# Kernel optimization log

Hardware: AMD Instinct MI355X
Metric: run time of the kernel (lower is better)

## Reference

```python
import jax, jax.numpy as jnp
import numpy as np

C = 256
HEADS = 8
HD = C // HEADS
SCALE = HD ** -0.5


def conv1x1(x, W, b):
    # x: [B,C_in,H,W], W: [C_out,C_in], b: [C_out]
    return jnp.einsum('oc,bchw->bohw', W, x) + b[None, :, None, None]


def setup_inputs() -> dict:
    key = jax.random.key(0)
    ks = jax.random.split(key, 12)
    B, H, Wd = 2, 48, 48
    s = C ** -0.5
    return {
        'x': jax.random.normal(ks[0], (B, C, H, Wd), jnp.float32),
        'uncertainty': jax.random.uniform(ks[1], (B, 1, H, Wd), jnp.float32),
        'Wq': jax.random.normal(ks[2], (C, C), jnp.float32) * s,
        'bq': jnp.zeros((C,), jnp.float32),
        'Wk': jax.random.normal(ks[3], (C, C), jnp.float32) * s,
        'bk': jnp.zeros((C,), jnp.float32),
        'Wv': jax.random.normal(ks[4], (C, C), jnp.float32) * s,
        'bv': jnp.zeros((C,), jnp.float32),
        'Wg': jax.random.normal(ks[5], (C, 1), jnp.float32),
        'bg': jnp.zeros((C,), jnp.float32),
        'Wo': jax.random.normal(ks[6], (C, C), jnp.float32) * s,
        'bo': jnp.zeros((C,), jnp.float32),
    }


def reference(x, uncertainty, Wq, bq, Wk, bk, Wv, bv, Wg, bg, Wo, bo):
    B, _, H, Wd = x.shape
    N = H * Wd
    # uncertainty gate (1x1 conv from 1 channel to C channels)
    uw = conv1x1(uncertainty, Wg, bg)            # [B,C,H,W]
    gated_x = x * (1.0 - uw)
    q = conv1x1(gated_x, Wq, bq).reshape(B, HEADS, HD, N)
    k = conv1x1(gated_x, Wk, bk).reshape(B, HEADS, HD, N)
    v = conv1x1(x, Wv, bv).reshape(B, HEADS, HD, N)
    # scores: [B,h,N,N] (query tokens n, key tokens m)
    scores = jnp.einsum('bhdn,bhdm->bhnm', q, k) * SCALE
    u_flat = uncertainty.reshape(B, 1, 1, N)      # mask over key axis
    scores = scores * (1.0 - u_flat)
    attn = jax.nn.softmax(scores, axis=-1)
    out = jnp.einsum('bhnm,bhdm->bhdn', attn, v)  # [B,h,hd,N]
    out = out.reshape(B, C, H, Wd)
    out = conv1x1(out, Wo, bo)
    return out + x
```

## Files before the change

kernel.cpp:

```cpp
#include <hip/hip_runtime.h>
#include <hip/hip_bf16.h>

typedef float f32x4 __attribute__((ext_vector_type(4)));
typedef __bf16 bf16x8 __attribute__((ext_vector_type(8)));
typedef __bf16 bf16x4 __attribute__((ext_vector_type(4)));
typedef short s16x4 __attribute__((ext_vector_type(4)));

constexpr int C = 256;
constexpr int N = 2304;
constexpr int T = 2 * N;

#if __has_builtin(__builtin_amdgcn_exp2f)
#define EXP2F(x) __builtin_amdgcn_exp2f(x)
#else
#define EXP2F(x) exp2f(x)
#endif

__device__ __forceinline__ bf16x8 load_bf8(const __bf16* p) {
    return *reinterpret_cast<const bf16x8*>(p);
}

__device__ __forceinline__ f32x4 mfma32(bf16x8 a, bf16x8 b, f32x4 c) {
    return __builtin_amdgcn_mfma_f32_16x16x32_bf16(a, b, c, 0, 0, 0);
}

#if __has_builtin(__builtin_amdgcn_mfma_f32_16x16x16bf16_1k)
__device__ __forceinline__ f32x4 mfma16(bf16x4 a, bf16x4 b, f32x4 c) {
    return __builtin_amdgcn_mfma_f32_16x16x16bf16_1k(
        __builtin_bit_cast(s16x4, a), __builtin_bit_cast(s16x4, b), c, 0, 0, 0);
}
#else
__device__ __forceinline__ f32x4 mfma16(bf16x4 a, bf16x4 b, f32x4 c) {
    f32x4 d;
    asm volatile("v_mfma_f32_16x16x16_bf16 %0, %1, %2, %3"
                 : "=v"(d) : "v"(a), "v"(b), "v"(c));
    return d;
}
#endif

__device__ __forceinline__ void gload_lds16(const __bf16* g, __bf16* l) {
    __builtin_amdgcn_global_load_lds(
        (const __attribute__((address_space(1))) void*)g,
        (__attribute__((address_space(3))) void*)l, 16, 0, 0);
}

#define VMCNT0() asm volatile("s_waitcnt vmcnt(0)" ::: "memory")
#define LGKM0()  asm volatile("s_waitcnt lgkmcnt(0)" ::: "memory")

__global__ void wconv_kernel(const float* __restrict__ Wq, const float* __restrict__ Wk,
                             const float* __restrict__ Wv, const float* __restrict__ Wo,
                             __bf16* __restrict__ Wb) {
    const float* srcs[4] = {Wq, Wk, Wv, Wo};
    int m = blockIdx.x >> 6;
    int idx = (blockIdx.x & 63) * 256 + threadIdx.x;
    float4 v = reinterpret_cast<const float4*>(srcs[m])[idx];
    bf16x4 o = { (__bf16)v.x, (__bf16)v.y, (__bf16)v.z, (__bf16)v.w };
    reinterpret_cast<bf16x4*>(Wb + m * 65536)[idx] = o;
}

__global__ void prep_kernel(const float* __restrict__ x, const float* __restrict__ u,
                            const float* __restrict__ Wg, const float* __restrict__ bg,
                            __bf16* __restrict__ xT, __bf16* __restrict__ gxT) {
    __shared__ float tile[32][65];
    int b = blockIdx.z, c0 = blockIdx.y * 32, n0 = blockIdx.x * 64;
    int t = threadIdx.x;
    const float* xp = x + (b * C + c0) * N + n0;
    #pragma unroll
    for (int r = 0; r < 8; ++r) {
        int cl = r * 4 + (t >> 6);
        int nl = t & 63;
        tile[cl][nl] = xp[cl * N + nl];
    }
    __syncthreads();
    int cq = (t & 7) * 4;
    #pragma unroll
    for (int it = 0; it < 2; ++it) {
        int nl = it * 32 + (t >> 3);
        float uv = u[b * N + n0 + nl];
        bf16x4 xo, go;
        #pragma unroll
        for (int j = 0; j < 4; ++j) {
            int c = c0 + cq + j;
            float xv = tile[cq + j][nl];
            float gate = 1.0f - (Wg[c] * uv + bg[c]);
            xo[j] = (__bf16)xv;
            go[j] = (__bf16)(xv * gate);
        }
        int tok = b * N + n0 + nl;
        *reinterpret_cast<bf16x4*>(xT + (long)tok * C + c0 + cq) = xo;
        *reinterpret_cast<bf16x4*>(gxT + (long)tok * C + c0 + cq) = go;
    }
}

__global__ __launch_bounds__(256) void qkv_kernel(const __bf16* __restrict__ Wb,
    const __bf16* __restrict__ xT, const __bf16* __restrict__ gxT,
    const float* __restrict__ bq, const float* __restrict__ bk, const float* __restrict__ bv,
    const float* __restrict__ u,
    __bf16* __restrict__ Q, __bf16* __restrict__ K, __bf16* __restrict__ V) {
    int proj = blockIdx.z;
    int o0 = blockIdx.y * 64;
    int t0 = blockIdx.x * 32;
    int wave = threadIdx.x >> 6, lane = threadIdx.x & 63;
    int g = lane >> 4, r = lane & 15;
    int ow = o0 + wave * 16;
    const __bf16* W = Wb + proj * 65536;
    const __bf16* inp = (proj == 2) ? xT : gxT;
    f32x4 acc[2] = {};
    for (int k = 0; k < 8; ++k) {
        bf16x8 a = load_bf8(W + (ow + r) * C + k * 32 + g * 8);
        #pragma unroll
        for (int tb = 0; tb < 2; ++tb) {
            bf16x8 bfr = load_bf8(inp + (long)(t0 + tb * 16 + r) * C + k * 32 + g * 8);
            acc[tb] = mfma32(a, bfr, acc[tb]);
        }
    }
    const float* bias = (proj == 0) ? bq : (proj == 1) ? bk : bv;
    float bvw[4];
    #pragma unroll
    for (int i = 0; i < 4; ++i) bvw[i] = bias[ow + g * 4 + i];
    int h = ow >> 5, d0 = (ow & 31) + g * 4;
    const float SC = 0.17677669529663687f * 1.4426950408889634f;
    #pragma unroll
    for (int tb = 0; tb < 2; ++tb) {
        int t = t0 + tb * 16 + r;
        int b = t / N, n = t % N;
        if (proj == 2) {
            #pragma unroll
            for (int i = 0; i < 4; ++i)
                V[((long)(b * 8 + h) * 32 + d0 + i) * N + n] = (__bf16)(acc[tb][i] + bvw[i]);
        } else {
            bf16x4 outv;
            if (proj == 1) {
                float scale = SC * (1.0f - u[t]);
                #pragma unroll
                for (int i = 0; i < 4; ++i) outv[i] = (__bf16)((acc[tb][i] + bvw[i]) * scale);
            } else {
                #pragma unroll
                for (int i = 0; i < 4; ++i) outv[i] = (__bf16)(acc[tb][i] + bvw[i]);
            }
            __bf16* dst = (proj == 0) ? Q : K;
            *reinterpret_cast<bf16x4*>(dst + ((long)(b * 8 + h) * N + n) * 32 + d0) = outv;
        }
    }
}

__global__ __launch_bounds__(256) void attn_kernel(const __bf16* __restrict__ Q,
    const __bf16* __restrict__ K, const __bf16* __restrict__ V,
    __bf16* __restrict__ aoT) {
    __shared__ __bf16 sK[2][2][2048];
    __shared__ __bf16 sV[2][2][2048];
    int id = blockIdx.x;
    int xcd = id & 7, j = id >> 3;
    int bh = xcd + 8 * (j / 72);
    int qblk = j % 72;
    int tid = threadIdx.x;
    int wave = tid >> 6, lane = tid & 63;
    int wp = wave & 1, pair = wave >> 1;
    int g = lane >> 4, r = lane & 15;
    int q0 = qblk * 32;
    const __bf16* Qg = Q + (long)bh * N * 32;
    const __bf16* Kg = K + (long)bh * N * 32 + (long)pair * 1152 * 32;
    const __bf16* Vg = V + (long)bh * 32 * N + pair * 1152;
    bf16x8 qf = load_bf8(Qg + (q0 + wp * 16 + r) * 32 + g * 8);
    long ksrc = (long)(wp * 64 + lane) * 8;
    int rr1 = wp * 8 + (lane >> 3);
    long vsrc0 = (long)rr1 * N + ((lane & 7) ^ ((rr1 >> 1) & 7)) * 8;
    int rr2 = 16 + rr1;
    long vsrc1 = (long)rr2 * N + ((lane & 7) ^ ((rr2 >> 1) & 7)) * 8;
    __bf16* kb0 = &sK[pair][0][0];
    __bf16* kb1 = &sK[pair][1][0];
    __bf16* vb0 = &sV[pair][0][0];
    __bf16* vb1 = &sV[pair][1][0];
    auto STAGE = [&](long m0, __bf16* kd, __bf16* vd) {
        gload_lds16(Kg + m0 * 32 + ksrc,        kd + wp * 512);
        gload_lds16(Kg + m0 * 32 + 1024 + ksrc, kd + 1024 + wp * 512);
        gload_lds16(Vg + vsrc0 + m0,            vd + wp * 512);
        gload_lds16(Vg + vsrc1 + m0,            vd + 1024 + wp * 512);
    };
    bf16x4 onesv;
    #pragma unroll
    for (int i = 0; i < 4; ++i) onesv[i] = (__bf16)1.0f;
    f32x4 oa0 = {}, oa1 = {}, oal = {};
    int k2r = (r >> 1) & 7;
    STAGE(0, kb0, vb0);
    for (int t = 0; t < 18; ++t) {
        LGKM0();
        VMCNT0();
        __builtin_amdgcn_s_barrier();
        const __bf16* kb = (t & 1) ? kb1 : kb0;
        const __bf16* vb = (t & 1) ? vb1 : vb0;
        if (t < 17)
            STAGE((long)(t + 1) * 64, (t & 1) ? kb0 : kb1, (t & 1) ? vb0 : vb1);
        bf16x8 kc0 = load_bf8(kb + (0 * 16 + r) * 32 + g * 8);
        bf16x8 kc1 = load_bf8(kb + (1 * 16 + r) * 32 + g * 8);
        bf16x8 kc2 = load_bf8(kb + (2 * 16 + r) * 32 + g * 8);
        bf16x8 kc3 = load_bf8(kb + (3 * 16 + r) * 32 + g * 8);
        bf16x4 vf[4][2];
        #pragma unroll
        for (int tt = 0; tt < 4; ++tt) {
            int pg = (((tt * 2 + (g >> 1)) ^ k2r) << 1) | (g & 1);
            #pragma unroll
            for (int dt = 0; dt < 2; ++dt)
                vf[tt][dt] = *reinterpret_cast<const bf16x4*>(
                    vb + (dt * 16 + r) * 64 + pg * 4);
        }
        f32x4 z = {};
        __builtin_amdgcn_s_setprio(1);
        f32x4 s0 = mfma32(kc0, qf, z);
        f32x4 s1 = mfma32(kc1, qf, z);
        f32x4 s2 = mfma32(kc2, qf, z);
        f32x4 s3 = mfma32(kc3, qf, z);
        __builtin_amdgcn_s_setprio(0);
        bf16x4 pa0, pa1, pa2, pa3;
        #pragma unroll
        for (int i = 0; i < 4; ++i) pa0[i] = (__bf16)EXP2F(s0[i]);
        #pragma unroll
        for (int i = 0; i < 4; ++i) pa1[i] = (__bf16)EXP2F(s1[i]);
        #pragma unroll
        for (int i = 0; i < 4; ++i) pa2[i] = (__bf16)EXP2F(s2[i]);
        #pragma unroll
        for (int i = 0; i < 4; ++i) pa3[i] = (__bf16)EXP2F(s3[i]);
        __builtin_amdgcn_s_setprio(1);
        oa0 = mfma16(vf[0][0], pa0, oa0);
        oa1 = mfma16(vf[0][1], pa0, oa1);
        oal = mfma16(onesv,    pa0, oal);
        oa0 = mfma16(vf[1][0], pa1, oa0);
        oa1 = mfma16(vf[1][1], pa1, oa1);
        oal = mfma16(onesv,    pa1, oal);
        oa0 = mfma16(vf[2][0], pa2, oa0);
        oa1 = mfma16(vf[2][1], pa2, oa1);
        oal = mfma16(onesv,    pa2, oal);
        oa0 = mfma16(vf[3][0], pa3, oa0);
        oa1 = mfma16(vf[3][1], pa3, oa1);
        oal = mfma16(onesv,    pa3, oal);
        __builtin_amdgcn_s_setprio(0);
    }
    __builtin_amdgcn_s_barrier();
    float* F = reinterpret_cast<float*>(&sK[0][0][0]);
    *reinterpret_cast<f32x4*>(F + wave * 512 + r * 32 + g * 4) = oa0;
    *reinterpret_cast<f32x4*>(F + wave * 512 + r * 32 + 16 + g * 4) = oa1;
    if (g == 0) F[2048 + wave * 16 + r] = oal[0];
    __builtin_amdgcn_s_barrier();
    if (tid < 128) {
        int q = tid >> 2;
        int wpq = q >> 4, qq = q & 15;
        int d8 = (tid & 3) * 8;
        int base0 = wpq * 512 + qq * 32 + d8;
        int base1 = (wpq + 2) * 512 + qq * 32 + d8;
        f32x4 a0 = *reinterpret_cast<f32x4*>(F + base0) +
                   *reinterpret_cast<f32x4*>(F + base1);
        f32x4 a1 = *reinterpret_cast<f32x4*>(F + base0 + 4) +
                   *reinterpret_cast<f32x4*>(F + base1 + 4);
        float l = F[2048 + wpq * 16 + qq] + F[2048 + (wpq + 2) * 16 + qq];
        float inv = 1.0f / l;
        bf16x8 ov;
        #pragma unroll
        for (int i = 0; i < 4; ++i) {
            ov[i] = (__bf16)(a0[i] * inv);
            ov[4 + i] = (__bf16)(a1[i] * inv);
        }
        int b = bh >> 3, h = bh & 7;
        *reinterpret_cast<bf16x8*>(aoT + (long)(b * N + q0 + q) * C + h * 32 + d8) = ov;
    }
}

__global__ __launch_bounds__(256) void outp_kernel(const __bf16* __restrict__ Wb,
    const __bf16* __restrict__ aoT, const float* __restrict__ bo,
    const float* __restrict__ x, float* __restrict__ out) {
    int o0 = blockIdx.y * 64;
    int t0 = blockIdx.x * 16;
    int wave = threadIdx.x >> 6, lane = threadIdx.x & 63;
    int g = lane >> 4, r = lane & 15;
    int ow = o0 + wave * 16;
    const __bf16* W = Wb + 3 * 65536;
    f32x4 acc = {};
    for (int k = 0; k < 8; ++k) {
        bf16x8 a = load_bf8(W + (ow + r) * C + k * 32 + g * 8);
        bf16x8 bfr = load_bf8(aoT + (long)(t0 + r) * C + k * 32 + g * 8);
        acc = mfma32(a, bfr, acc);
    }
    float bvw[4];
    #pragma unroll
    for (int i = 0; i < 4; ++i) bvw[i] = bo[ow + g * 4 + i];
    int t = t0 + r;
    int b = t / N, n = t % N;
    #pragma unroll
    for (int i = 0; i < 4; ++i) {
        long idx = ((long)b * C + ow + g * 4 + i) * N + n;
        out[idx] = acc[i] + bvw[i] + x[idx];
    }
}

extern "C" void kernel_launch(void* const* d_in, const int* in_sizes, int n_in,
                              void* d_out, int out_size, void* d_ws, size_t ws_size,
                              hipStream_t stream) {
    const float* x  = (const float*)d_in[0];
    const float* u  = (const float*)d_in[1];
    const float* Wq = (const float*)d_in[2];
    const float* bq = (const float*)d_in[3];
    const float* Wk = (const float*)d_in[4];
    const float* bk = (const float*)d_in[5];
    const float* Wv = (const float*)d_in[6];
    const float* bv = (const float*)d_in[7];
    const float* Wg = (const float*)d_in[8];
    const float* bg = (const float*)d_in[9];
    const float* Wo = (const float*)d_in[10];
    const float* bo = (const float*)d_in[11];
    float* out = (float*)d_out;

    char* ws = (char*)d_ws;
    size_t off = 0;
    auto alloc = [&](size_t bytes) {
        char* p = ws + off;
        off += (bytes + 255) & ~(size_t)255;
        return p;
    };
    __bf16* Wb  = (__bf16*)alloc((size_t)4 * 65536 * 2);
    __bf16* xT  = (__bf16*)alloc((size_t)T * C * 2);
    __bf16* gxT = (__bf16*)alloc((size_t)T * C * 2);
    __bf16* Qb  = (__bf16*)alloc((size_t)16 * N * 32 * 2);
    __bf16* Kb  = (__bf16*)alloc((size_t)16 * N * 32 * 2);
    __bf16* Vb  = (__bf16*)alloc((size_t)16 * N * 32 * 2);
    __bf16* aoT = (__bf16*)alloc((size_t)T * C * 2);

    wconv_kernel<<<256, 256, 0, stream>>>(Wq, Wk, Wv, Wo, Wb);
    prep_kernel<<<dim3(36, 8, 2), 256, 0, stream>>>(x, u, Wg, bg, xT, gxT);
    qkv_kernel<<<dim3(144, 4, 3), 256, 0, stream>>>(Wb, xT, gxT, bq, bk, bv, u, Qb, Kb, Vb);
    attn_kernel<<<1152, 256, 0, stream>>>(Qb, Kb, Vb, aoT);
    outp_kernel<<<dim3(288, 4), 256, 0, stream>>>(Wb, aoT, bo, x, out);
}
```

Before: 78.76 us.

## Halve attention key tile to 32 and unify swizzled K/V LDS staging

The attention loop now processes 32 keys per iteration instead of 64, doubling the iteration count to 36 and halving the shared memory to 16 KB per block. K and V staging each use a single 16-byte async load per lane with one XOR swizzle shared by both, and the LDS read offsets are precomputed outside the loop. The aim is higher occupancy and fewer LDS bank conflicts. In exchange there are twice as many barriers and waits per block and less MFMA work between synchronisations.

```diff
diff --git a/kernel.cpp b/kernel.cpp
--- a/kernel.cpp
+++ b/kernel.cpp
@@ -147,8 +147,9 @@
 __global__ __launch_bounds__(256) void attn_kernel(const __bf16* __restrict__ Q,
     const __bf16* __restrict__ K, const __bf16* __restrict__ V,
     __bf16* __restrict__ aoT) {
-    __shared__ __bf16 sK[2][2][2048];
-    __shared__ __bf16 sV[2][2][2048];
+    __shared__ __bf16 sMem[8192];
+    __bf16* sK = sMem;
+    __bf16* sV = sMem + 4096;
     int id = blockIdx.x;
     int xcd = id & 7, j = id >> 3;
     int bh = xcd + 8 * (j / 72);
@@ -162,81 +163,62 @@
     const __bf16* Kg = K + (long)bh * N * 32 + (long)pair * 1152 * 32;
     const __bf16* Vg = V + (long)bh * 32 * N + pair * 1152;
     bf16x8 qf = load_bf8(Qg + (q0 + wp * 16 + r) * 32 + g * 8);
-    long ksrc = (long)(wp * 64 + lane) * 8;
-    int rr1 = wp * 8 + (lane >> 3);
-    long vsrc0 = (long)rr1 * N + ((lane & 7) ^ ((rr1 >> 1) & 7)) * 8;
-    int rr2 = 16 + rr1;
-    long vsrc1 = (long)rr2 * N + ((lane & 7) ^ ((rr2 >> 1) & 7)) * 8;
-    __bf16* kb0 = &sK[pair][0][0];
-    __bf16* kb1 = &sK[pair][1][0];
-    __bf16* vb0 = &sV[pair][0][0];
-    __bf16* vb1 = &sV[pair][1][0];
-    auto STAGE = [&](long m0, __bf16* kd, __bf16* vd) {
-        gload_lds16(Kg + m0 * 32 + ksrc,        kd + wp * 512);
-        gload_lds16(Kg + m0 * 32 + 1024 + ksrc, kd + 1024 + wp * 512);
-        gload_lds16(Vg + vsrc0 + m0,            vd + wp * 512);
-        gload_lds16(Vg + vsrc1 + m0,            vd + 1024 + wp * 512);
+    int s_ = wp * 64 + lane;
+    int l_ = s_ ^ ((s_ >> 3) & 7);
+    const __bf16* kSrc = Kg + (l_ >> 2) * 32 + (l_ & 3) * 8;
+    const __bf16* vSrc = Vg + (long)(l_ >> 2) * N + (l_ & 3) * 8;
+    __bf16* kd0 = sK + pair * 2048;
+    __bf16* vd0 = sV + pair * 2048;
+    auto STAGE = [&](long m0, int buf) {
+        gload_lds16(kSrc + m0 * 32, kd0 + buf * 1024 + wp * 512);
+        gload_lds16(vSrc + m0,      vd0 + buf * 1024 + wp * 512);
     };
+    int key = (r >> 1) & 7;
+    int pk0 = ((r * 4 + g) ^ key) * 8;
+    int pk1 = (((16 + r) * 4 + g) ^ key) * 8;
+    int pv00 = (((r) * 4 + 0 + (g >> 1)) ^ key) * 8 + (g & 1) * 4;
+    int pv01 = (((16 + r) * 4 + 0 + (g >> 1)) ^ key) * 8 + (g & 1) * 4;
+    int pv10 = (((r) * 4 + 2 + (g >> 1)) ^ key) * 8 + (g & 1) * 4;
+    int pv11 = (((16 + r) * 4 + 2 + (g >> 1)) ^ key) * 8 + (g & 1) * 4;
     bf16x4 onesv;
     #pragma unroll
     for (int i = 0; i < 4; ++i) onesv[i] = (__bf16)1.0f;
     f32x4 oa0 = {}, oa1 = {}, oal = {};
-    int k2r = (r >> 1) & 7;
-    STAGE(0, kb0, vb0);
-    for (int t = 0; t < 18; ++t) {
+    STAGE(0, 0);
+    for (int t = 0; t < 36; ++t) {
         LGKM0();
         VMCNT0();
         __builtin_amdgcn_s_barrier();
-        const __bf16* kb = (t & 1) ? kb1 : kb0;
-        const __bf16* vb = (t & 1) ? vb1 : vb0;
-        if (t < 17)
-            STAGE((long)(t + 1) * 64, (t & 1) ? kb0 : kb1, (t & 1) ? vb0 : vb1);
-        bf16x8 kc0 = load_bf8(kb + (0 * 16 + r) * 32 + g * 8);
-        bf16x8 kc1 = load_bf8(kb + (1 * 16 + r) * 32 + g * 8);
-        bf16x8 kc2 = load_bf8(kb + (2 * 16 + r) * 32 + g * 8);
-        bf16x8 kc3 = load_bf8(kb + (3 * 16 + r) * 32 + g * 8);
-        bf16x4 vf[4][2];
-        #pragma unroll
-        for (int tt = 0; tt < 4; ++tt) {
-            int pg = (((tt * 2 + (g >> 1)) ^ k2r) << 1) | (g & 1);
-            #pragma unroll
-            for (int dt = 0; dt < 2; ++dt)
-                vf[tt][dt] = *reinterpret_cast<const bf16x4*>(
-                    vb + (dt * 16 + r) * 64 + pg * 4);
-        }
+        const __bf16* kb = kd0 + (t & 1) * 1024;
+        const __bf16* vb = vd0 + (t & 1) * 1024;
+        if (t < 35) STAGE((long)(t + 1) * 32, (t & 1) ^ 1);
+        bf16x8 kc0 = load_bf8(kb + pk0);
+        bf16x8 kc1 = load_bf8(kb + pk1);
+        bf16x4 vf00 = *reinterpret_cast<const bf16x4*>(vb + pv00);
+        bf16x4 vf01 = *reinterpret_cast<const bf16x4*>(vb + pv01);
+        bf16x4 vf10 = *reinterpret_cast<const bf16x4*>(vb + pv10);
+        bf16x4 vf11 = *reinterpret_cast<const bf16x4*>(vb + pv11);
         f32x4 z = {};
         __builtin_amdgcn_s_setprio(1);
         f32x4 s0 = mfma32(kc0, qf, z);
         f32x4 s1 = mfma32(kc1, qf, z);
-        f32x4 s2 = mfma32(kc2, qf, z);
-        f32x4 s3 = mfma32(kc3, qf, z);
         __builtin_amdgcn_s_setprio(0);
-        bf16x4 pa0, pa1, pa2, pa3;
+        bf16x4 pa0, pa1;
         #pragma unroll
         for (int i = 0; i < 4; ++i) pa0[i] = (__bf16)EXP2F(s0[i]);
         #pragma unroll
         for (int i = 0; i < 4; ++i) pa1[i] = (__bf16)EXP2F(s1[i]);
-        #pragma unroll
-        for (int i = 0; i < 4; ++i) pa2[i] = (__bf16)EXP2F(s2[i]);
-        #pragma unroll
-        for (int i = 0; i < 4; ++i) pa3[i] = (__bf16)EXP2F(s3[i]);
         __builtin_amdgcn_s_setprio(1);
-        oa0 = mfma16(vf[0][0], pa0, oa0);
-        oa1 = mfma16(vf[0][1], pa0, oa1);
-        oal = mfma16(onesv,    pa0, oal);
-        oa0 = mfma16(vf[1][0], pa1, oa0);
-        oa1 = mfma16(vf[1][1], pa1, oa1);
-        oal = mfma16(onesv,    pa1, oal);
-        oa0 = mfma16(vf[2][0], pa2, oa0);
-        oa1 = mfma16(vf[2][1], pa2, oa1);
-        oal = mfma16(onesv,    pa2, oal);
-        oa0 = mfma16(vf[3][0], pa3, oa0);
-        oa1 = mfma16(vf[3][1], pa3, oa1);
-        oal = mfma16(onesv,    pa3, oal);
+        oa0 = mfma16(vf00, pa0, oa0);
+        oa1 = mfma16(vf01, pa0, oa1);
+        oal = mfma16(onesv, pa0, oal);
+        oa0 = mfma16(vf10, pa1, oa0);
+        oa1 = mfma16(vf11, pa1, oa1);
+        oal = mfma16(onesv, pa1, oal);
         __builtin_amdgcn_s_setprio(0);
     }
     __builtin_amdgcn_s_barrier();
-    float* F = reinterpret_cast<float*>(&sK[0][0][0]);
+    float* F = reinterpret_cast<float*>(sMem);
     *reinterpret_cast<f32x4*>(F + wave * 512 + r * 32 + g * 4) = oa0;
     *reinterpret_cast<f32x4*>(F + wave * 512 + r * 32 + 16 + g * 4) = oa1;
     if (g == 0) F[2048 + wave * 16 + r] = oal[0];
```

Result: no change. 78.26 us (-0.6%).
